# Optimization experiments

Measured on AMD Instinct MI355X. Metric: run time of the kernel, lower is better.

## Reference

```python
import jax, jax.numpy as jnp
import numpy as np

N_NODES = 100000
N_EDGES = 625000
D = 128


def setup_inputs() -> dict:
    key = jax.random.key(0)
    ks = jax.random.split(key, 5)
    x = jax.random.normal(ks[0], (N_NODES, D), dtype=jnp.float32)
    edge_index = jax.random.randint(ks[1], (2, N_EDGES), 0, N_NODES, dtype=jnp.int64)
    scale = 1.0 / np.sqrt(D)
    W_neigh = jax.random.normal(ks[2], (D, D), dtype=jnp.float32) * scale
    W_self = jax.random.normal(ks[3], (D, D), dtype=jnp.float32) * scale
    b_self = jax.random.normal(ks[4], (D,), dtype=jnp.float32) * scale
    return {"x": x, "edge_index": edge_index, "W_neigh": W_neigh,
            "W_self": W_self, "b_self": b_self}


def reference(x, edge_index, W_neigh, W_self, b_self):
    src, dst = edge_index[0], edge_index[1]
    n = x.shape[0]
    # mean aggregation over incoming neighbors: segment-sum of x[src] into dst
    neigh = jax.ops.segment_sum(x[src], dst, num_segments=n)  # [N, D]
    counts = jax.ops.segment_sum(jnp.ones((src.shape[0],), dtype=x.dtype), dst,
                                 num_segments=n)  # [N]
    neigh = neigh / jnp.maximum(counts, 1.0)[:, None]
    # lin_self(x) + lin_neigh(neigh); nn.Linear computes x @ W.T + b
    return x @ W_self.T + b_self + neigh @ W_neigh.T
```

## Files before the change

kernel.cpp:

```cpp
#include <hip/hip_runtime.h>
#include <hip/hip_bf16.h>
#include <stdint.h>

#define DFEAT 128
#define CAP 40

typedef __attribute__((ext_vector_type(8))) short short8;
typedef __attribute__((ext_vector_type(4))) float f32x4;

static __device__ __forceinline__ unsigned short f2bf(float f) {
    union { float f; uint32_t u; } v; v.f = f;
    uint32_t u = v.u;
    u += 0x7FFFu + ((u >> 16) & 1u);
    return (unsigned short)(u >> 16);
}

static __device__ __forceinline__ float lo_bf(uint32_t u) {
    union { uint32_t u; float f; } v; v.u = u << 16; return v.f;
}
static __device__ __forceinline__ float hi_bf(uint32_t u) {
    union { uint32_t u; float f; } v; v.u = u & 0xFFFF0000u; return v.f;
}

static __device__ __forceinline__ short8 pack8(const float4& a, const float4& b) {
    short8 r;
    r[0] = (short)f2bf(a.x); r[1] = (short)f2bf(a.y);
    r[2] = (short)f2bf(a.z); r[3] = (short)f2bf(a.w);
    r[4] = (short)f2bf(b.x); r[5] = (short)f2bf(b.y);
    r[6] = (short)f2bf(b.z); r[7] = (short)f2bf(b.w);
    return r;
}

__global__ __launch_bounds__(256) void sage_prep(
    const float* __restrict__ x, unsigned short* __restrict__ xb, int total8,
    const int* __restrict__ ei, int* __restrict__ cur, int* __restrict__ nbr,
    int E) {
    int i = blockIdx.x * 256 + threadIdx.x;
    if (i < E) {
        int s = ei[i];
        int d = ei[E + i];
        int slot = atomicAdd(&cur[d], 1);
        if (slot < CAP) nbr[d * CAP + slot] = s;
    }
    if (i < total8) {
        float4 a = ((const float4*)x)[2 * i];
        float4 b = ((const float4*)x)[2 * i + 1];
        ((short8*)xb)[i] = pack8(a, b);
    }
}

__global__ __launch_bounds__(256) void sage_gather(
    const unsigned short* __restrict__ xb, const int* __restrict__ cur,
    const int* __restrict__ nbr, unsigned short* __restrict__ accb, int N) {
    int t = threadIdx.x;
    int wave = t >> 6;
    int lane = t & 63;
    int grp = lane >> 4;
    int sl = lane & 15;
    int node = blockIdx.x * 16 + wave * 4 + grp;
    if (node >= N) return;

    int degTrue = cur[node];
    int deg = degTrue < CAP ? degTrue : CAP;
    const int* nb = nbr + (size_t)node * CAP;

    float acc[8] = {0.f, 0.f, 0.f, 0.f, 0.f, 0.f, 0.f, 0.f};

    for (int j0 = 0; j0 < deg; j0 += 8) {
        int last = deg - 1;
        int idx[8];
        #pragma unroll
        for (int k = 0; k < 8; ++k) {
            int jj = j0 + k;
            idx[k] = nb[jj < deg ? jj : last];
        }
        uint4 u[8];
        #pragma unroll
        for (int k = 0; k < 8; ++k)
            u[k] = ((const uint4*)(xb + (size_t)idx[k] * DFEAT))[sl];
        #pragma unroll
        for (int k = 0; k < 8; ++k) {
            if (j0 + k < deg) {
                acc[0] += lo_bf(u[k].x); acc[1] += hi_bf(u[k].x);
                acc[2] += lo_bf(u[k].y); acc[3] += hi_bf(u[k].y);
                acc[4] += lo_bf(u[k].z); acc[5] += hi_bf(u[k].z);
                acc[6] += lo_bf(u[k].w); acc[7] += hi_bf(u[k].w);
            }
        }
    }

    float inv = 1.0f / fmaxf((float)degTrue, 1.0f);
    uint4 o;
    o.x = (uint32_t)f2bf(acc[0] * inv) | ((uint32_t)f2bf(acc[1] * inv) << 16);
    o.y = (uint32_t)f2bf(acc[2] * inv) | ((uint32_t)f2bf(acc[3] * inv) << 16);
    o.z = (uint32_t)f2bf(acc[4] * inv) | ((uint32_t)f2bf(acc[5] * inv) << 16);
    o.w = (uint32_t)f2bf(acc[6] * inv) | ((uint32_t)f2bf(acc[7] * inv) << 16);
    ((uint4*)(accb + (size_t)node * DFEAT))[sl] = o;
}

__global__ __launch_bounds__(256) void sage_gemm(
    const unsigned short* __restrict__ xb,
    const unsigned short* __restrict__ accb,
    const float* __restrict__ Ws,
    const float* __restrict__ Wn,
    const float* __restrict__ bias,
    float* __restrict__ out,
    int N, int numTiles) {
    __shared__ unsigned short wlds[128 * 256];

    int t = threadIdx.x;
    #pragma unroll
    for (int it = 0; it < 16; ++it) {
        int id = it * 256 + t;
        int n  = id >> 5;
        int c  = id & 31;
        const float* srcw = (c < 16) ? (Ws + n * 128 + c * 8)
                                     : (Wn + n * 128 + (c - 16) * 8);
        int cs = c ^ (n & 7);
        float4 u0 = *(const float4*)(srcw);
        float4 u1 = *(const float4*)(srcw + 4);
        *(short8*)(wlds + n * 256 + cs * 8) = pack8(u0, u1);
    }
    __syncthreads();

    int lane = t & 63;
    int wave = t >> 6;
    int m = lane & 15;
    int q = lane >> 4;

    for (int tile = blockIdx.x; tile < numTiles; tile += gridDim.x) {
        int arow = tile * 64 + wave * 16 + m;
        bool valid = arow < N;

        short8 afrag[8];
        if (valid) {
            const unsigned short* xr = xb   + (size_t)arow * DFEAT;
            const unsigned short* ar = accb + (size_t)arow * DFEAT;
            #pragma unroll
            for (int tt = 0; tt < 4; ++tt) {
                afrag[tt]     = *(const short8*)(xr + tt * 32 + q * 8);
                afrag[4 + tt] = *(const short8*)(ar + tt * 32 + q * 8);
            }
        } else {
            #pragma unroll
            for (int tt = 0; tt < 8; ++tt) {
                short8 z = {0, 0, 0, 0, 0, 0, 0, 0};
                afrag[tt] = z;
            }
        }

        int orow_base = tile * 64 + wave * 16 + q * 4;
        #pragma unroll
        for (int jt = 0; jt < 8; ++jt) {
            f32x4 c4 = {0.f, 0.f, 0.f, 0.f};
            int n = jt * 16 + m;
            #pragma unroll
            for (int tt = 0; tt < 8; ++tt) {
                int c = tt * 4 + q;
                int cs = c ^ (n & 7);
                short8 bfrag = *(const short8*)(wlds + n * 256 + cs * 8);
                c4 = __builtin_amdgcn_mfma_f32_16x16x32_bf16(afrag[tt], bfrag, c4, 0, 0, 0);
            }
            float bv = bias[n];
            #pragma unroll
            for (int r = 0; r < 4; ++r) {
                int orow = orow_base + r;
                if (orow < N) out[(size_t)orow * DFEAT + n] = c4[r] + bv;
            }
        }
    }
}

extern "C" void kernel_launch(void* const* d_in, const int* in_sizes, int n_in,
                              void* d_out, int out_size, void* d_ws, size_t ws_size,
                              hipStream_t stream) {
    const float* x  = (const float*)d_in[0];
    const int*   ei = (const int*)d_in[1];
    const float* Wn = (const float*)d_in[2];
    const float* Ws = (const float*)d_in[3];
    const float* b  = (const float*)d_in[4];
    float* out = (float*)d_out;

    int N = in_sizes[0] / DFEAT;
    int E = in_sizes[1] / 2;

    int* cur = (int*)d_ws;
    int* nbr = cur + N;
    unsigned short* xbuf = (unsigned short*)(nbr + (size_t)N * CAP);
    unsigned short* accb = xbuf + (size_t)N * DFEAT;

    hipMemsetAsync(cur, 0, (size_t)N * sizeof(int), stream);

    int total8 = N * DFEAT / 8;
    int prepThreads = total8 > E ? total8 : E;
    sage_prep<<<(prepThreads + 255) / 256, 256, 0, stream>>>(
        x, xbuf, total8, ei, cur, nbr, E);
    sage_gather<<<(N + 15) / 16, 256, 0, stream>>>(xbuf, cur, nbr, accb, N);

    int numTiles = (N + 63) / 64;
    sage_gemm<<<512, 256, 0, stream>>>(xbuf, accb, Ws, Wn, b, out, N, numTiles);
}
```

Baseline: 192.1 us.

## Split prep into edge and convert blocks, pad counters, use nontemporal memory ops

```diff
diff --git a/kernel.cpp b/kernel.cpp
--- a/kernel.cpp
+++ b/kernel.cpp
@@ -4,6 +4,7 @@
 
 #define DFEAT 128
 #define CAP 40
+#define CURSTRIDE 4
 
 typedef __attribute__((ext_vector_type(8))) short short8;
 typedef __attribute__((ext_vector_type(4))) float f32x4;
@@ -31,21 +32,44 @@
     return r;
 }
 
+static __device__ __forceinline__ short8 pack8v(const f32x4& a, const f32x4& b) {
+    short8 r;
+    r[0] = (short)f2bf(a[0]); r[1] = (short)f2bf(a[1]);
+    r[2] = (short)f2bf(a[2]); r[3] = (short)f2bf(a[3]);
+    r[4] = (short)f2bf(b[0]); r[5] = (short)f2bf(b[1]);
+    r[6] = (short)f2bf(b[2]); r[7] = (short)f2bf(b[3]);
+    return r;
+}
+
 __global__ __launch_bounds__(256) void sage_prep(
     const float* __restrict__ x, unsigned short* __restrict__ xb, int total8,
     const int* __restrict__ ei, int* __restrict__ cur, int* __restrict__ nbr,
-    int E) {
-    int i = blockIdx.x * 256 + threadIdx.x;
-    if (i < E) {
-        int s = ei[i];
-        int d = ei[E + i];
-        int slot = atomicAdd(&cur[d], 1);
-        if (slot < CAP) nbr[d * CAP + slot] = s;
-    }
-    if (i < total8) {
-        float4 a = ((const float4*)x)[2 * i];
-        float4 b = ((const float4*)x)[2 * i + 1];
-        ((short8*)xb)[i] = pack8(a, b);
+    int E, int EH, int edgeBlocks) {
+    int bid = blockIdx.x;
+    if (bid < edgeBlocks) {
+        int et = bid * 256 + threadIdx.x;
+        if (et < EH) {
+            int e0 = et;
+            int e1 = et + EH;
+            bool has1 = e1 < E;
+            int s0 = ei[e0];
+            int d0 = ei[E + e0];
+            int s1 = 0, d1 = 0;
+            if (has1) { s1 = ei[e1]; d1 = ei[E + e1]; }
+            int slot0 = atomicAdd(&cur[d0 * CURSTRIDE], 1);
+            int slot1 = has1 ? atomicAdd(&cur[d1 * CURSTRIDE], 1) : CAP;
+            if (slot0 < CAP) nbr[(size_t)d0 * CAP + slot0] = s0;
+            if (has1 && slot1 < CAP) nbr[(size_t)d1 * CAP + slot1] = s1;
+        }
+    } else {
+        int i = (bid - edgeBlocks) * 256 + threadIdx.x;
+        if (i < total8) {
+            const f32x4* xp = (const f32x4*)x;
+            f32x4 a = __builtin_nontemporal_load(&xp[2 * i]);
+            f32x4 b = __builtin_nontemporal_load(&xp[2 * i + 1]);
+            short8 r = pack8v(a, b);
+            __builtin_nontemporal_store(r, &((short8*)xb)[i]);
+        }
     }
 }
 
@@ -60,7 +84,7 @@
     int node = blockIdx.x * 16 + wave * 4 + grp;
     if (node >= N) return;
 
-    int degTrue = cur[node];
+    int degTrue = cur[node * CURSTRIDE];
     int deg = degTrue < CAP ? degTrue : CAP;
     const int* nb = nbr + (size_t)node * CAP;
 
@@ -165,7 +189,9 @@
             #pragma unroll
             for (int r = 0; r < 4; ++r) {
                 int orow = orow_base + r;
-                if (orow < N) out[(size_t)orow * DFEAT + n] = c4[r] + bv;
+                if (orow < N)
+                    __builtin_nontemporal_store(c4[r] + bv,
+                                                &out[(size_t)orow * DFEAT + n]);
             }
         }
     }
@@ -185,16 +211,18 @@
     int E = in_sizes[1] / 2;
 
     int* cur = (int*)d_ws;
-    int* nbr = cur + N;
+    int* nbr = cur + (size_t)N * CURSTRIDE;
     unsigned short* xbuf = (unsigned short*)(nbr + (size_t)N * CAP);
     unsigned short* accb = xbuf + (size_t)N * DFEAT;
 
-    hipMemsetAsync(cur, 0, (size_t)N * sizeof(int), stream);
+    hipMemsetAsync(cur, 0, (size_t)N * CURSTRIDE * sizeof(int), stream);
 
     int total8 = N * DFEAT / 8;
-    int prepThreads = total8 > E ? total8 : E;
-    sage_prep<<<(prepThreads + 255) / 256, 256, 0, stream>>>(
-        x, xbuf, total8, ei, cur, nbr, E);
+    int EH = (E + 1) / 2;
+    int edgeBlocks = (EH + 255) / 256;
+    int convBlocks = (total8 + 255) / 256;
+    sage_prep<<<edgeBlocks + convBlocks, 256, 0, stream>>>(
+        x, xbuf, total8, ei, cur, nbr, E, EH, edgeBlocks);
     sage_gather<<<(N + 15) / 16, 256, 0, stream>>>(xbuf, cur, nbr, accb, N);
 
     int numTiles = (N + 63) / 64;
```

Measured after the change: 197.3 us. 1.03x slower.

## Fuse neighbor gather into GEMM kernel via LDS staging of mean features

Applied to the files above, without the earlier changes.

```diff
diff --git a/kernel.cpp b/kernel.cpp
--- a/kernel.cpp
+++ b/kernel.cpp
@@ -49,64 +49,17 @@
     }
 }
 
-__global__ __launch_bounds__(256) void sage_gather(
-    const unsigned short* __restrict__ xb, const int* __restrict__ cur,
-    const int* __restrict__ nbr, unsigned short* __restrict__ accb, int N) {
-    int t = threadIdx.x;
-    int wave = t >> 6;
-    int lane = t & 63;
-    int grp = lane >> 4;
-    int sl = lane & 15;
-    int node = blockIdx.x * 16 + wave * 4 + grp;
-    if (node >= N) return;
-
-    int degTrue = cur[node];
-    int deg = degTrue < CAP ? degTrue : CAP;
-    const int* nb = nbr + (size_t)node * CAP;
-
-    float acc[8] = {0.f, 0.f, 0.f, 0.f, 0.f, 0.f, 0.f, 0.f};
-
-    for (int j0 = 0; j0 < deg; j0 += 8) {
-        int last = deg - 1;
-        int idx[8];
-        #pragma unroll
-        for (int k = 0; k < 8; ++k) {
-            int jj = j0 + k;
-            idx[k] = nb[jj < deg ? jj : last];
-        }
-        uint4 u[8];
-        #pragma unroll
-        for (int k = 0; k < 8; ++k)
-            u[k] = ((const uint4*)(xb + (size_t)idx[k] * DFEAT))[sl];
-        #pragma unroll
-        for (int k = 0; k < 8; ++k) {
-            if (j0 + k < deg) {
-                acc[0] += lo_bf(u[k].x); acc[1] += hi_bf(u[k].x);
-                acc[2] += lo_bf(u[k].y); acc[3] += hi_bf(u[k].y);
-                acc[4] += lo_bf(u[k].z); acc[5] += hi_bf(u[k].z);
-                acc[6] += lo_bf(u[k].w); acc[7] += hi_bf(u[k].w);
-            }
-        }
-    }
-
-    float inv = 1.0f / fmaxf((float)degTrue, 1.0f);
-    uint4 o;
-    o.x = (uint32_t)f2bf(acc[0] * inv) | ((uint32_t)f2bf(acc[1] * inv) << 16);
-    o.y = (uint32_t)f2bf(acc[2] * inv) | ((uint32_t)f2bf(acc[3] * inv) << 16);
-    o.z = (uint32_t)f2bf(acc[4] * inv) | ((uint32_t)f2bf(acc[5] * inv) << 16);
-    o.w = (uint32_t)f2bf(acc[6] * inv) | ((uint32_t)f2bf(acc[7] * inv) << 16);
-    ((uint4*)(accb + (size_t)node * DFEAT))[sl] = o;
-}
-
-__global__ __launch_bounds__(256) void sage_gemm(
+__global__ __launch_bounds__(256) void sage_fused(
     const unsigned short* __restrict__ xb,
-    const unsigned short* __restrict__ accb,
+    const int* __restrict__ cur,
+    const int* __restrict__ nbr,
     const float* __restrict__ Ws,
     const float* __restrict__ Wn,
     const float* __restrict__ bias,
     float* __restrict__ out,
     int N, int numTiles) {
     __shared__ unsigned short wlds[128 * 256];
+    __shared__ unsigned short nlds[64 * 128];
 
     int t = threadIdx.x;
     #pragma unroll
@@ -127,26 +80,76 @@
     int wave = t >> 6;
     int m = lane & 15;
     int q = lane >> 4;
+    int grp = wave * 4 + q;
+    int sl = lane & 15;
 
     for (int tile = blockIdx.x; tile < numTiles; tile += gridDim.x) {
+        #pragma unroll
+        for (int k = 0; k < 4; ++k) {
+            int rl = grp + k * 16;
+            int node = tile * 64 + rl;
+            float acc[8] = {0.f, 0.f, 0.f, 0.f, 0.f, 0.f, 0.f, 0.f};
+            int degTrue = 0;
+            if (node < N) {
+                degTrue = cur[node];
+                int deg = degTrue < CAP ? degTrue : CAP;
+                const int* nb = nbr + (size_t)node * CAP;
+                for (int j0 = 0; j0 < deg; j0 += 8) {
+                    int last = deg - 1;
+                    int idx[8];
+                    #pragma unroll
+                    for (int kk = 0; kk < 8; ++kk) {
+                        int jj = j0 + kk;
+                        idx[kk] = nb[jj < deg ? jj : last];
+                    }
+                    uint4 u[8];
+                    #pragma unroll
+                    for (int kk = 0; kk < 8; ++kk)
+                        u[kk] = ((const uint4*)(xb + (size_t)idx[kk] * DFEAT))[sl];
+                    #pragma unroll
+                    for (int kk = 0; kk < 8; ++kk) {
+                        if (j0 + kk < deg) {
+                            acc[0] += lo_bf(u[kk].x); acc[1] += hi_bf(u[kk].x);
+                            acc[2] += lo_bf(u[kk].y); acc[3] += hi_bf(u[kk].y);
+                            acc[4] += lo_bf(u[kk].z); acc[5] += hi_bf(u[kk].z);
+                            acc[6] += lo_bf(u[kk].w); acc[7] += hi_bf(u[kk].w);
+                        }
+                    }
+                }
+            }
+            float inv = 1.0f / fmaxf((float)degTrue, 1.0f);
+            uint4 o;
+            o.x = (uint32_t)f2bf(acc[0] * inv) | ((uint32_t)f2bf(acc[1] * inv) << 16);
+            o.y = (uint32_t)f2bf(acc[2] * inv) | ((uint32_t)f2bf(acc[3] * inv) << 16);
+            o.z = (uint32_t)f2bf(acc[4] * inv) | ((uint32_t)f2bf(acc[5] * inv) << 16);
+            o.w = (uint32_t)f2bf(acc[6] * inv) | ((uint32_t)f2bf(acc[7] * inv) << 16);
+            int us = sl ^ (rl & 7);
+            *(uint4*)(nlds + rl * 128 + us * 8) = o;
+        }
+        __syncthreads();
+
         int arow = tile * 64 + wave * 16 + m;
         bool valid = arow < N;
 
         short8 afrag[8];
         if (valid) {
-            const unsigned short* xr = xb   + (size_t)arow * DFEAT;
-            const unsigned short* ar = accb + (size_t)arow * DFEAT;
+            const unsigned short* xr = xb + (size_t)arow * DFEAT;
+            #pragma unroll
+            for (int tt = 0; tt < 4; ++tt)
+                afrag[tt] = *(const short8*)(xr + tt * 32 + q * 8);
+        } else {
             #pragma unroll
             for (int tt = 0; tt < 4; ++tt) {
-                afrag[tt]     = *(const short8*)(xr + tt * 32 + q * 8);
-                afrag[4 + tt] = *(const short8*)(ar + tt * 32 + q * 8);
-            }
-        } else {
-            #pragma unroll
-            for (int tt = 0; tt < 8; ++tt) {
                 short8 z = {0, 0, 0, 0, 0, 0, 0, 0};
                 afrag[tt] = z;
             }
+        }
+        int rloc = wave * 16 + m;
+        #pragma unroll
+        for (int tt = 0; tt < 4; ++tt) {
+            int u = tt * 4 + q;
+            int us = u ^ (m & 7);
+            afrag[4 + tt] = *(const short8*)(nlds + rloc * 128 + us * 8);
         }
 
         int orow_base = tile * 64 + wave * 16 + q * 4;
@@ -168,6 +171,7 @@
                 if (orow < N) out[(size_t)orow * DFEAT + n] = c4[r] + bv;
             }
         }
+        __syncthreads();
     }
 }
 
@@ -187,7 +191,6 @@
     int* cur = (int*)d_ws;
     int* nbr = cur + N;
     unsigned short* xbuf = (unsigned short*)(nbr + (size_t)N * CAP);
-    unsigned short* accb = xbuf + (size_t)N * DFEAT;
 
     hipMemsetAsync(cur, 0, (size_t)N * sizeof(int), stream);
 
@@ -195,8 +198,7 @@
     int prepThreads = total8 > E ? total8 : E;
     sage_prep<<<(prepThreads + 255) / 256, 256, 0, stream>>>(
         x, xbuf, total8, ei, cur, nbr, E);
-    sage_gather<<<(N + 15) / 16, 256, 0, stream>>>(xbuf, cur, nbr, accb, N);
 
     int numTiles = (N + 63) / 64;
-    sage_gemm<<<512, 256, 0, stream>>>(xbuf, accb, Ws, Wn, b, out, N, numTiles);
-}
+    sage_fused<<<512, 256, 0, stream>>>(xbuf, cur, nbr, Ws, Wn, b, out, N, numTiles);
+}
```

After: 208.5 us. +8.5%, slower.

## Split prep kernel into vectorized edge blocks and strided conversion blocks

Applied to the files above, without the earlier changes.

```diff
diff --git a/kernel.cpp b/kernel.cpp
--- a/kernel.cpp
+++ b/kernel.cpp
@@ -34,18 +34,49 @@
 __global__ __launch_bounds__(256) void sage_prep(
     const float* __restrict__ x, unsigned short* __restrict__ xb, int total8,
     const int* __restrict__ ei, int* __restrict__ cur, int* __restrict__ nbr,
-    int E) {
-    int i = blockIdx.x * 256 + threadIdx.x;
-    if (i < E) {
-        int s = ei[i];
-        int d = ei[E + i];
-        int slot = atomicAdd(&cur[d], 1);
-        if (slot < CAP) nbr[d * CAP + slot] = s;
-    }
-    if (i < total8) {
-        float4 a = ((const float4*)x)[2 * i];
-        float4 b = ((const float4*)x)[2 * i + 1];
-        ((short8*)xb)[i] = pack8(a, b);
+    int E, int EQ, int edgeBlocks) {
+    int bid = blockIdx.x;
+    if (bid < edgeBlocks) {
+        int t = bid * 256 + threadIdx.x;
+        if (t < EQ) {
+            int4 s4 = ((const int4*)ei)[t];
+            int4 d4 = ((const int4*)(ei + E))[t];
+            int sl0 = atomicAdd(&cur[d4.x], 1);
+            int sl1 = atomicAdd(&cur[d4.y], 1);
+            int sl2 = atomicAdd(&cur[d4.z], 1);
+            int sl3 = atomicAdd(&cur[d4.w], 1);
+            if (sl0 < CAP) nbr[(size_t)d4.x * CAP + sl0] = s4.x;
+            if (sl1 < CAP) nbr[(size_t)d4.y * CAP + sl1] = s4.y;
+            if (sl2 < CAP) nbr[(size_t)d4.z * CAP + sl2] = s4.z;
+            if (sl3 < CAP) nbr[(size_t)d4.w * CAP + sl3] = s4.w;
+        }
+        if (t == 0) {
+            for (int e = EQ * 4; e < E; ++e) {
+                int s = ei[e];
+                int d = ei[E + e];
+                int slot = atomicAdd(&cur[d], 1);
+                if (slot < CAP) nbr[(size_t)d * CAP + slot] = s;
+            }
+        }
+    } else {
+        int stride = (gridDim.x - edgeBlocks) * 256;
+        for (int i = (bid - edgeBlocks) * 256 + threadIdx.x; i < total8;
+             i += stride * 4) {
+            float4 a[4], b[4];
+            #pragma unroll
+            for (int k = 0; k < 4; ++k) {
+                int j = i + k * stride;
+                if (j < total8) {
+                    a[k] = ((const float4*)x)[2 * j];
+                    b[k] = ((const float4*)x)[2 * j + 1];
+                }
+            }
+            #pragma unroll
+            for (int k = 0; k < 4; ++k) {
+                int j = i + k * stride;
+                if (j < total8) ((short8*)xb)[j] = pack8(a[k], b[k]);
+            }
+        }
     }
 }
 
@@ -192,9 +223,12 @@
     hipMemsetAsync(cur, 0, (size_t)N * sizeof(int), stream);
 
     int total8 = N * DFEAT / 8;
-    int prepThreads = total8 > E ? total8 : E;
-    sage_prep<<<(prepThreads + 255) / 256, 256, 0, stream>>>(
-        x, xbuf, total8, ei, cur, nbr, E);
+    int EQ = E >> 2;
+    int edgeBlocks = (EQ + 255) / 256;
+    int convBlocks = 1024;
+    sage_prep<<<edgeBlocks + convBlocks, 256, 0, stream>>>(
+        x, xbuf, total8, ei, cur, nbr, E, EQ, edgeBlocks);
+
     sage_gather<<<(N + 15) / 16, 256, 0, stream>>>(xbuf, cur, nbr, accb, N);
 
     int numTiles = (N + 63) / 64;
```

Measured after the change: 190.8 us, median of 2. No clear change (-0.7%).
